# Kernel tuning notes

Hardware: AMD Instinct MI355X
Metric: run time of the kernel (lower is better)

## Reference

```python
import jax, jax.numpy as jnp
from jax import lax
import numpy as np

B, T, F_IN = 64, 3072, 128
CONV_OUT, K, STRIDE = 64, 3, 3
HID, OUT = 256, 10


def setup_inputs() -> dict:
    key = jax.random.key(0)
    ks = jax.random.split(key, 10)
    s = 0.05
    return {
        "input": jax.random.normal(ks[0], (B, T, F_IN), jnp.float32),
        "r": jnp.zeros(((T - K) // STRIDE + 1, B, CONV_OUT), jnp.float32),
        "hx0": jax.random.normal(ks[1], (B, HID), jnp.float32),
        "cx0": jax.random.normal(ks[2], (B, HID), jnp.float32),
        "conv_w": jax.random.normal(ks[3], (CONV_OUT, F_IN, K), jnp.float32) * s,
        "conv_b": jnp.zeros((CONV_OUT,), jnp.float32),
        "w_ih": jax.random.normal(ks[4], (4 * HID, CONV_OUT), jnp.float32) * s,
        "b_ih": jnp.zeros((4 * HID,), jnp.float32),
        "w_hh": jax.random.normal(ks[5], (4 * HID, HID), jnp.float32) * s,
        "b_hh": jnp.zeros((4 * HID,), jnp.float32),
        "lin_w": jax.random.normal(ks[6], (OUT, HID), jnp.float32) * s,
        "lin_b": jnp.zeros((OUT,), jnp.float32),
        "batch_size": B,
    }


def reference(input, r, hx0, cx0, conv_w, conv_b, w_ih, b_ih, w_hh, b_hh, lin_w, lin_b, batch_size):
    # F.normalize: L2 normalize along dim=1 (the time dim), eps=1e-12
    norm = jnp.sqrt(jnp.sum(input * input, axis=1, keepdims=True))
    x = input / jnp.maximum(norm, 1e-12)
    x = jnp.transpose(x, (0, 2, 1))  # [B, F_IN, T]
    x = lax.conv_general_dilated(
        x, conv_w, window_strides=(STRIDE,), padding='VALID',
        dimension_numbers=('NCH', 'OIH', 'NCH')) + conv_b[None, :, None]
    x = jax.nn.relu(x)
    x = jnp.transpose(x, (2, 0, 1))  # [T', B, 64]

    def step(carry, xt):
        h, c = carry
        gates = xt @ w_ih.T + b_ih + h @ w_hh.T + b_hh  # [B, 4H]
        i, f, g, o = jnp.split(gates, 4, axis=-1)
        c = jax.nn.sigmoid(f) * c + jax.nn.sigmoid(i) * jnp.tanh(g)
        h = jax.nn.sigmoid(o) * jnp.tanh(c)
        return (h, c), None

    (h, _), _ = lax.scan(step, (hx0, cx0), x)
    return h @ lin_w.T + lin_b  # [B, OUT]
```

## Files before the change

kernel.cpp:

```cpp
#include <hip/hip_runtime.h>
#include <math.h>

#define B_N 64
#define T_N 3072
#define FIN 128
#define TP 1024
#define COUT 64
#define HID 256
#define G4 1024
#define OUT_N 10
#define NCHUNK 24
#define CHUNK_T (T_N / NCHUNK)

#define WREG 24
#define WLDS 8

typedef _Float16 h2_t __attribute__((ext_vector_type(2)));
typedef unsigned u32x4 __attribute__((ext_vector_type(4)));

#if defined(__has_builtin)
#if __has_builtin(__builtin_amdgcn_fdot2)
#define HAVE_FDOT2 1
#endif
#endif

__device__ __forceinline__ float fdot2(unsigned w, unsigned h, float acc) {
#ifdef HAVE_FDOT2
    return __builtin_amdgcn_fdot2(__builtin_bit_cast(h2_t, w),
                                  __builtin_bit_cast(h2_t, h), acc, false);
#else
    h2_t wv = __builtin_bit_cast(h2_t, w), hv = __builtin_bit_cast(h2_t, h);
    return acc + (float)wv.x * (float)hv.x + (float)wv.y * (float)hv.y;
#endif
}

__device__ __forceinline__ unsigned pack2(float a, float b) {
    unsigned la = (unsigned)__builtin_bit_cast(unsigned short, (_Float16)a);
    unsigned lb = (unsigned)__builtin_bit_cast(unsigned short, (_Float16)b);
    return la | (lb << 16);
}

__global__ void pack_weights(const float* __restrict__ w_ih,
                             const float* __restrict__ w_hh,
                             unsigned* __restrict__ whhR,
                             unsigned* __restrict__ whhL,
                             float* __restrict__ wihT) {
    int col = blockIdx.x, d = threadIdx.x;
    const float* wr = w_hh + col * HID;
    unsigned p = pack2(wr[2 * d], wr[2 * d + 1]);
    int c = d >> 2, r = d & 3;
    if (c < WREG) whhR[(c * 1024 + col) * 4 + r] = p;
    else          whhL[((c - WREG) * 1024 + col) * 4 + r] = p;
    if (d < COUT) wihT[d * 1024 + col] = w_ih[col * COUT + d];
}

__global__ void prep_conv_w(const float* __restrict__ conv_w, float* __restrict__ wc2) {
    int i = blockIdx.x * 256 + threadIdx.x;
    if (i < 24576) {
        int j = i >> 6, oc = i & 63;
        int kk = j >> 7, ic = j & 127;
        wc2[i] = conv_w[(oc * 128 + ic) * 3 + kk];
    }
}

__global__ void norm_partial(const float* __restrict__ in, float* __restrict__ part) {
    int b = blockIdx.x, ch = blockIdx.y, f = threadIdx.x;
    const float* p = in + ((size_t)b * T_N + (size_t)ch * CHUNK_T) * FIN + f;
    float s0 = 0.f, s1 = 0.f, s2 = 0.f, s3 = 0.f;
#pragma unroll
    for (int r = 0; r < CHUNK_T; r += 4) {
        float v0 = p[(r + 0) * FIN];
        float v1 = p[(r + 1) * FIN];
        float v2 = p[(r + 2) * FIN];
        float v3 = p[(r + 3) * FIN];
        s0 += v0 * v0; s1 += v1 * v1; s2 += v2 * v2; s3 += v3 * v3;
    }
    part[(b * NCHUNK + ch) * FIN + f] = (s0 + s1) + (s2 + s3);
}

__global__ __launch_bounds__(256) void conv_relu(
        const float* __restrict__ in, const float* __restrict__ part,
        const float* __restrict__ wc2, const float* __restrict__ cb,
        float* __restrict__ X) {
    __shared__ __align__(16) float xs[16 * 384];
    __shared__ __align__(16) float wsh[96 * 64];
    __shared__ float invn[FIN];

    int b = blockIdx.x, tile = blockIdx.y;
    int tid = threadIdx.x;

    if (tid < FIN) {
        float s = 0.f;
#pragma unroll
        for (int c = 0; c < NCHUNK; c++) s += part[(b * NCHUNK + c) * FIN + tid];
        invn[tid] = rsqrtf(fmaxf(s, 1e-24f));
    }
    __syncthreads();

    const float* ip = in + ((size_t)b * T_N + (size_t)tile * 48) * FIN;
    for (int i = tid; i < 6144; i += 256) xs[i] = ip[i] * invn[i & 127];

    int oc = tid & 63, tq = tid >> 6;
    float acc0 = 0.f, acc1 = 0.f, acc2 = 0.f, acc3 = 0.f;
    const float* xb = xs + tq * 4 * 384;

    for (int c = 0; c < 4; c++) {
        __syncthreads();
        for (int i = tid; i < 6144; i += 256) wsh[i] = wc2[c * 6144 + i];
        __syncthreads();
#pragma unroll 8
        for (int jj = 0; jj < 96; jj += 4) {
            int j = c * 96 + jj;
            float w0 = wsh[(jj + 0) * 64 + oc];
            float w1 = wsh[(jj + 1) * 64 + oc];
            float w2 = wsh[(jj + 2) * 64 + oc];
            float w3 = wsh[(jj + 3) * 64 + oc];
            float4 x0 = *(const float4*)(xb + j);
            float4 x1 = *(const float4*)(xb + 384 + j);
            float4 x2 = *(const float4*)(xb + 768 + j);
            float4 x3 = *(const float4*)(xb + 1152 + j);
            acc0 += w0 * x0.x + w1 * x0.y + w2 * x0.z + w3 * x0.w;
            acc1 += w0 * x1.x + w1 * x1.y + w2 * x1.z + w3 * x1.w;
            acc2 += w0 * x2.x + w1 * x2.y + w2 * x2.z + w3 * x2.w;
            acc3 += w0 * x3.x + w1 * x3.y + w2 * x3.z + w3 * x3.w;
        }
    }
    float bb = cb[oc];
    int tp0 = tile * 16 + tq * 4;
    size_t o = ((size_t)b * TP + tp0) * COUT + oc;
    X[o]       = fmaxf(acc0 + bb, 0.f);
    X[o + 64]  = fmaxf(acc1 + bb, 0.f);
    X[o + 128] = fmaxf(acc2 + bb, 0.f);
    X[o + 192] = fmaxf(acc3 + bb, 0.f);
}

__global__ __launch_bounds__(256) void x_gemm(
        const float* __restrict__ X, const float* __restrict__ wihT,
        const float* __restrict__ b_ih, const float* __restrict__ b_hh,
        _Float16* __restrict__ xg) {
    __shared__ float xs[64 * 17];
    int b = blockIdx.x, t0 = blockIdx.y * 16, tid = threadIdx.x;

    const float* Xp = X + ((size_t)b * TP + t0) * COUT;
    for (int i = tid; i < 1024; i += 256) {
        int r = i >> 6, k = i & 63;
        xs[k * 17 + r] = Xp[i];
    }
    __syncthreads();

#pragma unroll
    for (int jt = 0; jt < 4; jt++) {
        int jj = jt * 256 + tid;
        float bias = b_ih[jj] + b_hh[jj];
        float acc[16];
#pragma unroll
        for (int r = 0; r < 16; r++) acc[r] = bias;
        for (int k = 0; k < 64; k++) {
            float w = wihT[k * 1024 + jj];
#pragma unroll
            for (int r = 0; r < 16; r++) acc[r] += w * xs[k * 17 + r];
        }
#pragma unroll
        for (int r = 0; r < 16; r++)
            xg[((size_t)b * TP + t0 + r) * 1024 + jj] = (_Float16)acc[r];
    }
}

__device__ __forceinline__ float fsig(float x) {
    return 1.f / (1.f + __expf(-x));
}
__device__ __forceinline__ float ftanh(float x) {
    float xc = fminf(fmaxf(x, -15.f), 15.f);
    float e = __expf(2.f * xc);
    return (e - 1.f) / (e + 1.f);
}

#define SM_WL   0
#define SM_H    131072
#define SM_FO   131584
#define SM_H32  133632
#define SM_SIZE 134656

#define REP24(M) M(0) M(1) M(2) M(3) M(4) M(5) M(6) M(7) M(8) M(9) M(10) M(11) \
                 M(12) M(13) M(14) M(15) M(16) M(17) M(18) M(19) M(20) M(21) M(22) M(23)
#define REP8(M)  M(0) M(1) M(2) M(3) M(4) M(5) M(6) M(7)

#define DECLW(n)  u32x4 wa##n, wb##n;
#define LOADW(n)  wa##n = whhR4[(n) * 1024 + j]; wb##n = whhR4[(n) * 1024 + j + 512];
#define DOTCH(n)  { u32x4 H = hs4[n]; \
    a0 = fdot2(wa##n[0], H[0], a0); a1 = fdot2(wb##n[0], H[0], a1); \
    a0 = fdot2(wa##n[1], H[1], a0); a1 = fdot2(wb##n[1], H[1], a1); \
    a0 = fdot2(wa##n[2], H[2], a0); a1 = fdot2(wb##n[2], H[2], a1); \
    a0 = fdot2(wa##n[3], H[3], a0); a1 = fdot2(wb##n[3], H[3], a1); }
#define DOTLDS(m) { u32x4 WA = wL[(m) * 1024 + j]; u32x4 WB = wL[(m) * 1024 + j + 512]; \
    u32x4 H = hs4[WREG + (m)]; \
    a0 = fdot2(WA[0], H[0], a0); a1 = fdot2(WB[0], H[0], a1); \
    a0 = fdot2(WA[1], H[1], a0); a1 = fdot2(WB[1], H[1], a1); \
    a0 = fdot2(WA[2], H[2], a0); a1 = fdot2(WB[2], H[2], a1); \
    a0 = fdot2(WA[3], H[3], a0); a1 = fdot2(WB[3], H[3], a1); }

__global__ __attribute__((amdgpu_flat_work_group_size(512, 512),
                          amdgpu_waves_per_eu(2, 2)))
void lstm_kernel(
        const u32x4* __restrict__ whhR4, const u32x4* __restrict__ whhL4,
        const _Float16* __restrict__ xg,
        const float* __restrict__ hx0, const float* __restrict__ cx0,
        const float* __restrict__ lin_w, const float* __restrict__ lin_b,
        float* __restrict__ out) {
    extern __shared__ char smem[];
    u32x4*    wL    = (u32x4*)(smem + SM_WL);
    _Float16* h_s   = (_Float16*)(smem + SM_H);
    float2*   fo_s  = (float2*)(smem + SM_FO);
    float*    h32_s = (float*)(smem + SM_H32);

    const int b = blockIdx.x, j = threadIdx.x;

    REP24(DECLW)
    REP24(LOADW)

    for (int i = j; i < WLDS * 1024; i += 512) wL[i] = whhL4[i];

    float c_reg = 0.f;
    if (j < HID) {
        c_reg = cx0[b * HID + j];
        h_s[j] = (_Float16)hx0[b * HID + j];
    }
    const _Float16* Xg = xg + (size_t)b * TP * G4;
    _Float16 xa = Xg[j], xb = Xg[j + 512];
    __syncthreads();

    const u32x4* hs4 = (const u32x4*)h_s;

    for (int t = 0; t < TP; t++) {
        _Float16 xan = (_Float16)0.f, xbn = (_Float16)0.f;
        if (t + 1 < TP) {
            xan = Xg[(t + 1) * G4 + j];
            xbn = Xg[(t + 1) * G4 + j + 512];
        }

        float a0 = (float)xa, a1 = (float)xb;
        REP24(DOTCH)
        REP8(DOTLDS)

        float s0 = 0.f, s1 = 0.f;
        if (j >= HID) {
            fo_s[j - HID] = make_float2(fsig(a0), fsig(a1));
        } else {
            s0 = fsig(a0);
            s1 = ftanh(a1);
        }
        __syncthreads();
        if (j < HID) {
            float2 fo = fo_s[j];
            c_reg = fo.x * c_reg + s0 * s1;
            float hh = fo.y * ftanh(c_reg);
            h_s[j] = (_Float16)hh;
            if (t == TP - 1) h32_s[j] = hh;
        }
        __syncthreads();
        xa = xan; xb = xbn;
    }

    if (j < OUT_N) {
        float s = lin_b[j];
        const float* lw = lin_w + j * HID;
#pragma unroll 4
        for (int k = 0; k < HID; k++) s += h32_s[k] * lw[k];
        out[b * OUT_N + j] = s;
    }
}

extern "C" void kernel_launch(void* const* d_in, const int* in_sizes, int n_in,
                              void* d_out, int out_size, void* d_ws, size_t ws_size,
                              hipStream_t stream) {
    const float* input  = (const float*)d_in[0];
    const float* hx0    = (const float*)d_in[2];
    const float* cx0    = (const float*)d_in[3];
    const float* conv_w = (const float*)d_in[4];
    const float* conv_b = (const float*)d_in[5];
    const float* w_ih   = (const float*)d_in[6];
    const float* b_ih   = (const float*)d_in[7];
    const float* w_hh   = (const float*)d_in[8];
    const float* b_hh   = (const float*)d_in[9];
    const float* lin_w  = (const float*)d_in[10];
    const float* lin_b  = (const float*)d_in[11];

    float* ws = (float*)d_ws;
    float*     part = ws;
    float*     X    = part + 196608;
    float*     wc2  = X + 4194304;
    float*     wihT = wc2 + 24576;
    unsigned*  whhR = (unsigned*)(wihT + 65536);
    unsigned*  whhL = whhR + WREG * 1024 * 4;
    _Float16*  xg   = (_Float16*)(whhL + WLDS * 1024 * 4);

    (void)hipFuncSetAttribute((const void*)lstm_kernel,
                              hipFuncAttributeMaxDynamicSharedMemorySize, SM_SIZE);

    pack_weights<<<1024, 128, 0, stream>>>(w_ih, w_hh, whhR, whhL, wihT);
    prep_conv_w<<<96, 256, 0, stream>>>(conv_w, wc2);
    norm_partial<<<dim3(B_N, NCHUNK), FIN, 0, stream>>>(input, part);
    conv_relu<<<dim3(B_N, 64), 256, 0, stream>>>(input, part, wc2, conv_b, X);
    x_gemm<<<dim3(B_N, 64), 256, 0, stream>>>(X, wihT, b_ih, b_hh, xg);
    lstm_kernel<<<B_N, 512, SM_SIZE, stream>>>(
        (const u32x4*)whhR, (const u32x4*)whhL, xg,
        hx0, cx0, lin_w, lin_b, (float*)d_out);
}
```

Baseline: 2.527 ms.

## Use 1024 threads per LSTM block, one gate column per thread, three-tier weight storage

New measurement: 2.586 ms. 2.3% more time.

```diff
diff --git a/kernel.cpp b/kernel.cpp
--- a/kernel.cpp
+++ b/kernel.cpp
@@ -12,8 +12,9 @@
 #define NCHUNK 24
 #define CHUNK_T (T_N / NCHUNK)
 
-#define WREG 24
-#define WLDS 8
+#define CREG 20
+#define CLDS 9
+#define CSTR 3
 
 typedef _Float16 h2_t __attribute__((ext_vector_type(2)));
 typedef unsigned u32x4 __attribute__((ext_vector_type(4)));
@@ -44,13 +45,15 @@
                              const float* __restrict__ w_hh,
                              unsigned* __restrict__ whhR,
                              unsigned* __restrict__ whhL,
+                             unsigned* __restrict__ whhS,
                              float* __restrict__ wihT) {
     int col = blockIdx.x, d = threadIdx.x;
     const float* wr = w_hh + col * HID;
     unsigned p = pack2(wr[2 * d], wr[2 * d + 1]);
     int c = d >> 2, r = d & 3;
-    if (c < WREG) whhR[(c * 1024 + col) * 4 + r] = p;
-    else          whhL[((c - WREG) * 1024 + col) * 4 + r] = p;
+    if (c < CREG)            whhR[((c) * 1024 + col) * 4 + r] = p;
+    else if (c < CREG + CLDS) whhL[((c - CREG) * 1024 + col) * 4 + r] = p;
+    else                     whhS[((c - CREG - CLDS) * 1024 + col) * 4 + r] = p;
     if (d < COUT) wihT[d * 1024 + col] = w_ih[col * COUT + d];
 }
 
@@ -176,33 +179,27 @@
 }
 
 #define SM_WL   0
-#define SM_H    131072
-#define SM_FO   131584
-#define SM_H32  133632
-#define SM_SIZE 134656
-
-#define REP24(M) M(0) M(1) M(2) M(3) M(4) M(5) M(6) M(7) M(8) M(9) M(10) M(11) \
-                 M(12) M(13) M(14) M(15) M(16) M(17) M(18) M(19) M(20) M(21) M(22) M(23)
-#define REP8(M)  M(0) M(1) M(2) M(3) M(4) M(5) M(6) M(7)
-
-#define DECLW(n)  u32x4 wa##n, wb##n;
-#define LOADW(n)  wa##n = whhR4[(n) * 1024 + j]; wb##n = whhR4[(n) * 1024 + j + 512];
-#define DOTCH(n)  { u32x4 H = hs4[n]; \
-    a0 = fdot2(wa##n[0], H[0], a0); a1 = fdot2(wb##n[0], H[0], a1); \
-    a0 = fdot2(wa##n[1], H[1], a0); a1 = fdot2(wb##n[1], H[1], a1); \
-    a0 = fdot2(wa##n[2], H[2], a0); a1 = fdot2(wb##n[2], H[2], a1); \
-    a0 = fdot2(wa##n[3], H[3], a0); a1 = fdot2(wb##n[3], H[3], a1); }
-#define DOTLDS(m) { u32x4 WA = wL[(m) * 1024 + j]; u32x4 WB = wL[(m) * 1024 + j + 512]; \
-    u32x4 H = hs4[WREG + (m)]; \
-    a0 = fdot2(WA[0], H[0], a0); a1 = fdot2(WB[0], H[0], a1); \
-    a0 = fdot2(WA[1], H[1], a0); a1 = fdot2(WB[1], H[1], a1); \
-    a0 = fdot2(WA[2], H[2], a0); a1 = fdot2(WB[2], H[2], a1); \
-    a0 = fdot2(WA[3], H[3], a0); a1 = fdot2(WB[3], H[3], a1); }
-
-__global__ __attribute__((amdgpu_flat_work_group_size(512, 512),
-                          amdgpu_waves_per_eu(2, 2)))
+#define SM_H    147456
+#define SM_GSH  147968
+#define SM_H32  151040
+#define SM_SIZE 152064
+
+#define REP20(M) M(0) M(1) M(2) M(3) M(4) M(5) M(6) M(7) M(8) M(9) \
+                 M(10) M(11) M(12) M(13) M(14) M(15) M(16) M(17) M(18) M(19)
+#define REP9(M)  M(0) M(1) M(2) M(3) M(4) M(5) M(6) M(7) M(8)
+
+#define DECLW(n)  u32x4 wr##n;
+#define LOADW(n)  wr##n = whhR4[(n) * 1024 + j];
+#define DOT4(W, H) { \
+    a0 = fdot2((W)[0], (H)[0], a0); a0 = fdot2((W)[1], (H)[1], a0); \
+    a0 = fdot2((W)[2], (H)[2], a0); a0 = fdot2((W)[3], (H)[3], a0); }
+#define DOTCH(n)  { u32x4 H = hs4[n]; DOT4(wr##n, H); }
+#define DOTLDS(m) { u32x4 W = wL[(m) * 1024 + j]; u32x4 H = hs4[CREG + (m)]; DOT4(W, H); }
+
+__global__ __attribute__((amdgpu_flat_work_group_size(1024, 1024)))
 void lstm_kernel(
         const u32x4* __restrict__ whhR4, const u32x4* __restrict__ whhL4,
+        const u32x4* __restrict__ whhS4,
         const _Float16* __restrict__ xg,
         const float* __restrict__ hx0, const float* __restrict__ cx0,
         const float* __restrict__ lin_w, const float* __restrict__ lin_b,
@@ -210,15 +207,15 @@
     extern __shared__ char smem[];
     u32x4*    wL    = (u32x4*)(smem + SM_WL);
     _Float16* h_s   = (_Float16*)(smem + SM_H);
-    float2*   fo_s  = (float2*)(smem + SM_FO);
+    float*    gsh   = (float*)(smem + SM_GSH);
     float*    h32_s = (float*)(smem + SM_H32);
 
     const int b = blockIdx.x, j = threadIdx.x;
 
-    REP24(DECLW)
-    REP24(LOADW)
-
-    for (int i = j; i < WLDS * 1024; i += 512) wL[i] = whhL4[i];
+    REP20(DECLW)
+    REP20(LOADW)
+
+    for (int i = j; i < CLDS * 1024; i += 1024) wL[i] = whhL4[i];
 
     float c_reg = 0.f;
     if (j < HID) {
@@ -226,39 +223,43 @@
         h_s[j] = (_Float16)hx0[b * HID + j];
     }
     const _Float16* Xg = xg + (size_t)b * TP * G4;
-    _Float16 xa = Xg[j], xb = Xg[j + 512];
+    _Float16 xa = Xg[j];
     __syncthreads();
 
     const u32x4* hs4 = (const u32x4*)h_s;
+    const u32x4* sP = whhS4 + j;
 
     for (int t = 0; t < TP; t++) {
-        _Float16 xan = (_Float16)0.f, xbn = (_Float16)0.f;
-        if (t + 1 < TP) {
-            xan = Xg[(t + 1) * G4 + j];
-            xbn = Xg[(t + 1) * G4 + j + 512];
+        _Float16 xan = (_Float16)0.f;
+        if (t + 1 < TP) xan = Xg[(t + 1) * G4 + j];
+
+        u32x4 s0 = sP[0 * 1024], s1 = sP[1 * 1024], s2 = sP[2 * 1024];
+
+        float a0 = (float)xa;
+        REP20(DOTCH)
+        REP9(DOTLDS)
+        { u32x4 H = hs4[29]; DOT4(s0, H); }
+        { u32x4 H = hs4[30]; DOT4(s1, H); }
+        { u32x4 H = hs4[31]; DOT4(s2, H); }
+
+        if (j >= HID) {
+            float v;
+            if (j < 512)      v = fsig(a0);
+            else if (j < 768) v = ftanh(a0);
+            else              v = fsig(a0);
+            gsh[j - HID] = v;
         }
-
-        float a0 = (float)xa, a1 = (float)xb;
-        REP24(DOTCH)
-        REP8(DOTLDS)
-
-        float s0 = 0.f, s1 = 0.f;
-        if (j >= HID) {
-            fo_s[j - HID] = make_float2(fsig(a0), fsig(a1));
-        } else {
-            s0 = fsig(a0);
-            s1 = ftanh(a1);
-        }
+        float ig = fsig(a0);
         __syncthreads();
         if (j < HID) {
-            float2 fo = fo_s[j];
-            c_reg = fo.x * c_reg + s0 * s1;
-            float hh = fo.y * ftanh(c_reg);
+            float fg = gsh[j], gg = gsh[HID + j], og = gsh[2 * HID + j];
+            c_reg = fg * c_reg + ig * gg;
+            float hh = og * ftanh(c_reg);
             h_s[j] = (_Float16)hh;
             if (t == TP - 1) h32_s[j] = hh;
         }
         __syncthreads();
-        xa = xan; xb = xbn;
+        xa = xan;
     }
 
     if (j < OUT_N) {
@@ -291,18 +292,19 @@
     float*     wc2  = X + 4194304;
     float*     wihT = wc2 + 24576;
     unsigned*  whhR = (unsigned*)(wihT + 65536);
-    unsigned*  whhL = whhR + WREG * 1024 * 4;
-    _Float16*  xg   = (_Float16*)(whhL + WLDS * 1024 * 4);
+    unsigned*  whhL = whhR + CREG * 1024 * 4;
+    unsigned*  whhS = whhL + CLDS * 1024 * 4;
+    _Float16*  xg   = (_Float16*)(whhS + CSTR * 1024 * 4);
 
     (void)hipFuncSetAttribute((const void*)lstm_kernel,
                               hipFuncAttributeMaxDynamicSharedMemorySize, SM_SIZE);
 
-    pack_weights<<<1024, 128, 0, stream>>>(w_ih, w_hh, whhR, whhL, wihT);
+    pack_weights<<<1024, 128, 0, stream>>>(w_ih, w_hh, whhR, whhL, whhS, wihT);
     prep_conv_w<<<96, 256, 0, stream>>>(conv_w, wc2);
     norm_partial<<<dim3(B_N, NCHUNK), FIN, 0, stream>>>(input, part);
     conv_relu<<<dim3(B_N, 64), 256, 0, stream>>>(input, part, wc2, conv_b, X);
     x_gemm<<<dim3(B_N, 64), 256, 0, stream>>>(X, wihT, b_ih, b_hh, xg);
-    lstm_kernel<<<B_N, 512, SM_SIZE, stream>>>(
-        (const u32x4*)whhR, (const u32x4*)whhL, xg,
+    lstm_kernel<<<B_N, 1024, SM_SIZE, stream>>>(
+        (const u32x4*)whhR, (const u32x4*)whhL, (const u32x4*)whhS, xg,
         hx0, cx0, lin_w, lin_b, (float*)d_out);
 }
```

## Hold recurrent weights in AGPRs so W_hh splits VGPR/AGPR/LDS evenly

Applied to the files above, without the earlier changes.

Measured after the change: 3.030 ms. 19.9% more time.

```diff
diff --git a/kernel.cpp b/kernel.cpp
--- a/kernel.cpp
+++ b/kernel.cpp
@@ -12,8 +12,6 @@
 #define NCHUNK 24
 #define CHUNK_T (T_N / NCHUNK)
 
-#define WREG 24
-#define WLDS 8
 
 typedef _Float16 h2_t __attribute__((ext_vector_type(2)));
 typedef unsigned u32x4 __attribute__((ext_vector_type(4)));
@@ -42,15 +40,22 @@
 
 __global__ void pack_weights(const float* __restrict__ w_ih,
                              const float* __restrict__ w_hh,
-                             unsigned* __restrict__ whhR,
+                             unsigned* __restrict__ whhV,
+                             unsigned* __restrict__ whhA,
                              unsigned* __restrict__ whhL,
                              float* __restrict__ wihT) {
     int col = blockIdx.x, d = threadIdx.x;
     const float* wr = w_hh + col * HID;
     unsigned p = pack2(wr[2 * d], wr[2 * d + 1]);
     int c = d >> 2, r = d & 3;
-    if (c < WREG) whhR[(c * 1024 + col) * 4 + r] = p;
-    else          whhL[((c - WREG) * 1024 + col) * 4 + r] = p;
+    if (col < 512) {
+        if (c < 16) whhV[((c) * 512 + col) * 4 + r] = p;
+        else        whhA[((c - 16) * 512 + col) * 4 + r] = p;
+    } else {
+        int jj = col - 512;
+        if (c < 16) whhA[((16 + c) * 512 + jj) * 4 + r] = p;
+        else        whhL[((c - 16) * 512 + jj) * 4 + r] = p;
+    }
     if (d < COUT) wihT[d * 1024 + col] = w_ih[col * COUT + d];
 }
 
@@ -175,50 +180,76 @@
     return (e - 1.f) / (e + 1.f);
 }
 
-#define SM_WL   0
+#define SM_WLB  0
 #define SM_H    131072
 #define SM_FO   131584
 #define SM_H32  133632
 #define SM_SIZE 134656
 
-#define REP24(M) M(0) M(1) M(2) M(3) M(4) M(5) M(6) M(7) M(8) M(9) M(10) M(11) \
-                 M(12) M(13) M(14) M(15) M(16) M(17) M(18) M(19) M(20) M(21) M(22) M(23)
-#define REP8(M)  M(0) M(1) M(2) M(3) M(4) M(5) M(6) M(7)
-
-#define DECLW(n)  u32x4 wa##n, wb##n;
-#define LOADW(n)  wa##n = whhR4[(n) * 1024 + j]; wb##n = whhR4[(n) * 1024 + j + 512];
-#define DOTCH(n)  { u32x4 H = hs4[n]; \
-    a0 = fdot2(wa##n[0], H[0], a0); a1 = fdot2(wb##n[0], H[0], a1); \
-    a0 = fdot2(wa##n[1], H[1], a0); a1 = fdot2(wb##n[1], H[1], a1); \
-    a0 = fdot2(wa##n[2], H[2], a0); a1 = fdot2(wb##n[2], H[2], a1); \
-    a0 = fdot2(wa##n[3], H[3], a0); a1 = fdot2(wb##n[3], H[3], a1); }
-#define DOTLDS(m) { u32x4 WA = wL[(m) * 1024 + j]; u32x4 WB = wL[(m) * 1024 + j + 512]; \
-    u32x4 H = hs4[WREG + (m)]; \
-    a0 = fdot2(WA[0], H[0], a0); a1 = fdot2(WB[0], H[0], a1); \
-    a0 = fdot2(WA[1], H[1], a0); a1 = fdot2(WB[1], H[1], a1); \
-    a0 = fdot2(WA[2], H[2], a0); a1 = fdot2(WB[2], H[2], a1); \
-    a0 = fdot2(WA[3], H[3], a0); a1 = fdot2(WB[3], H[3], a1); }
-
-__global__ __attribute__((amdgpu_flat_work_group_size(512, 512),
-                          amdgpu_waves_per_eu(2, 2)))
-void lstm_kernel(
-        const u32x4* __restrict__ whhR4, const u32x4* __restrict__ whhL4,
+#define REP16(M) M(0) M(1) M(2) M(3) M(4) M(5) M(6) M(7) \
+                 M(8) M(9) M(10) M(11) M(12) M(13) M(14) M(15)
+
+#define DECLV(n)  u32x4 wr##n;
+#define LOADV(n)  wr##n = whhV4[(n) * 512 + j];
+#define PINV(n)   asm volatile("" : "+v"(wr##n));
+
+#define DECLAG(n) unsigned ag##n##_0, ag##n##_1, ag##n##_2, ag##n##_3, \
+                           bg##n##_0, bg##n##_1, bg##n##_2, bg##n##_3;
+#define INITAG(n) { u32x4 v = whhA4[(n) * 512 + j]; \
+    asm volatile("v_accvgpr_write_b32 %0, %1" : "=a"(ag##n##_0) : "v"(v[0])); \
+    asm volatile("v_accvgpr_write_b32 %0, %1" : "=a"(ag##n##_1) : "v"(v[1])); \
+    asm volatile("v_accvgpr_write_b32 %0, %1" : "=a"(ag##n##_2) : "v"(v[2])); \
+    asm volatile("v_accvgpr_write_b32 %0, %1" : "=a"(ag##n##_3) : "v"(v[3])); \
+    v = whhA4[(16 + (n)) * 512 + j]; \
+    asm volatile("v_accvgpr_write_b32 %0, %1" : "=a"(bg##n##_0) : "v"(v[0])); \
+    asm volatile("v_accvgpr_write_b32 %0, %1" : "=a"(bg##n##_1) : "v"(v[1])); \
+    asm volatile("v_accvgpr_write_b32 %0, %1" : "=a"(bg##n##_2) : "v"(v[2])); \
+    asm volatile("v_accvgpr_write_b32 %0, %1" : "=a"(bg##n##_3) : "v"(v[3])); }
+
+#define DOT_LO(n) { u32x4 H = hs4[n]; \
+    a0 = fdot2(wr##n[0], H[0], a0); a0 = fdot2(wr##n[1], H[1], a0); \
+    a0 = fdot2(wr##n[2], H[2], a0); a0 = fdot2(wr##n[3], H[3], a0); \
+    unsigned w0, w1, w2, w3; \
+    asm volatile("v_accvgpr_read_b32 %0, %1" : "=v"(w0) : "a"(bg##n##_0)); \
+    asm volatile("v_accvgpr_read_b32 %0, %1" : "=v"(w1) : "a"(bg##n##_1)); \
+    asm volatile("v_accvgpr_read_b32 %0, %1" : "=v"(w2) : "a"(bg##n##_2)); \
+    asm volatile("v_accvgpr_read_b32 %0, %1" : "=v"(w3) : "a"(bg##n##_3)); \
+    a1 = fdot2(w0, H[0], a1); a1 = fdot2(w1, H[1], a1); \
+    a1 = fdot2(w2, H[2], a1); a1 = fdot2(w3, H[3], a1); }
+
+#define DOT_HI(n) { u32x4 H = hs4[16 + (n)]; \
+    unsigned w0, w1, w2, w3; \
+    asm volatile("v_accvgpr_read_b32 %0, %1" : "=v"(w0) : "a"(ag##n##_0)); \
+    asm volatile("v_accvgpr_read_b32 %0, %1" : "=v"(w1) : "a"(ag##n##_1)); \
+    asm volatile("v_accvgpr_read_b32 %0, %1" : "=v"(w2) : "a"(ag##n##_2)); \
+    asm volatile("v_accvgpr_read_b32 %0, %1" : "=v"(w3) : "a"(ag##n##_3)); \
+    a0 = fdot2(w0, H[0], a0); a0 = fdot2(w1, H[1], a0); \
+    a0 = fdot2(w2, H[2], a0); a0 = fdot2(w3, H[3], a0); \
+    u32x4 W = wLB4[(n) * 512 + j]; \
+    a1 = fdot2(W[0], H[0], a1); a1 = fdot2(W[1], H[1], a1); \
+    a1 = fdot2(W[2], H[2], a1); a1 = fdot2(W[3], H[3], a1); }
+
+__global__ __launch_bounds__(512) void lstm_kernel(
+        const u32x4* __restrict__ whhV4, const u32x4* __restrict__ whhA4,
+        const u32x4* __restrict__ whhL4,
         const _Float16* __restrict__ xg,
         const float* __restrict__ hx0, const float* __restrict__ cx0,
         const float* __restrict__ lin_w, const float* __restrict__ lin_b,
         float* __restrict__ out) {
     extern __shared__ char smem[];
-    u32x4*    wL    = (u32x4*)(smem + SM_WL);
+    u32x4*    wLB4  = (u32x4*)(smem + SM_WLB);
     _Float16* h_s   = (_Float16*)(smem + SM_H);
     float2*   fo_s  = (float2*)(smem + SM_FO);
     float*    h32_s = (float*)(smem + SM_H32);
 
     const int b = blockIdx.x, j = threadIdx.x;
 
-    REP24(DECLW)
-    REP24(LOADW)
-
-    for (int i = j; i < WLDS * 1024; i += 512) wL[i] = whhL4[i];
+    REP16(DECLV)
+    REP16(LOADV)
+    REP16(PINV)
+    REP16(DECLAG)
+    REP16(INITAG)
+    for (int i = j; i < 16 * 512; i += 512) wLB4[i] = whhL4[i];
 
     float c_reg = 0.f;
     if (j < HID) {
@@ -226,39 +257,34 @@
         h_s[j] = (_Float16)hx0[b * HID + j];
     }
     const _Float16* Xg = xg + (size_t)b * TP * G4;
-    _Float16 xa = Xg[j], xb = Xg[j + 512];
+    _Float16 xa0 = Xg[j], xa1 = Xg[j + 512];
     __syncthreads();
 
     const u32x4* hs4 = (const u32x4*)h_s;
 
+#pragma unroll 1
     for (int t = 0; t < TP; t++) {
-        _Float16 xan = (_Float16)0.f, xbn = (_Float16)0.f;
+        _Float16 xn0 = (_Float16)0.f, xn1 = (_Float16)0.f;
         if (t + 1 < TP) {
-            xan = Xg[(t + 1) * G4 + j];
-            xbn = Xg[(t + 1) * G4 + j + 512];
+            xn0 = Xg[(t + 1) * G4 + j];
+            xn1 = Xg[(t + 1) * G4 + j + 512];
         }
 
-        float a0 = (float)xa, a1 = (float)xb;
-        REP24(DOTCH)
-        REP8(DOTLDS)
-
-        float s0 = 0.f, s1 = 0.f;
-        if (j >= HID) {
-            fo_s[j - HID] = make_float2(fsig(a0), fsig(a1));
-        } else {
-            s0 = fsig(a0);
-            s1 = ftanh(a1);
-        }
+        float a0 = (float)xa0, a1 = (float)xa1;
+        REP16(DOT_LO)
+        REP16(DOT_HI)
+
+        if (j >= HID) fo_s[j - HID] = make_float2(fsig(a0), fsig(a1));
         __syncthreads();
         if (j < HID) {
             float2 fo = fo_s[j];
-            c_reg = fo.x * c_reg + s0 * s1;
+            c_reg = fo.x * c_reg + fsig(a0) * ftanh(a1);
             float hh = fo.y * ftanh(c_reg);
             h_s[j] = (_Float16)hh;
             if (t == TP - 1) h32_s[j] = hh;
         }
         __syncthreads();
-        xa = xan; xb = xbn;
+        xa0 = xn0; xa1 = xn1;
     }
 
     if (j < OUT_N) {
@@ -290,19 +316,20 @@
     float*     X    = part + 196608;
     float*     wc2  = X + 4194304;
     float*     wihT = wc2 + 24576;
-    unsigned*  whhR = (unsigned*)(wihT + 65536);
-    unsigned*  whhL = whhR + WREG * 1024 * 4;
-    _Float16*  xg   = (_Float16*)(whhL + WLDS * 1024 * 4);
+    unsigned*  whhV = (unsigned*)(wihT + 65536);
+    unsigned*  whhA = whhV + 32768;
+    unsigned*  whhL = whhA + 65536;
+    _Float16*  xg   = (_Float16*)(whhL + 32768);
 
     (void)hipFuncSetAttribute((const void*)lstm_kernel,
                               hipFuncAttributeMaxDynamicSharedMemorySize, SM_SIZE);
 
-    pack_weights<<<1024, 128, 0, stream>>>(w_ih, w_hh, whhR, whhL, wihT);
+    pack_weights<<<1024, 128, 0, stream>>>(w_ih, w_hh, whhV, whhA, whhL, wihT);
     prep_conv_w<<<96, 256, 0, stream>>>(conv_w, wc2);
     norm_partial<<<dim3(B_N, NCHUNK), FIN, 0, stream>>>(input, part);
     conv_relu<<<dim3(B_N, 64), 256, 0, stream>>>(input, part, wc2, conv_b, X);
     x_gemm<<<dim3(B_N, 64), 256, 0, stream>>>(X, wihT, b_ih, b_hh, xg);
     lstm_kernel<<<B_N, 512, SM_SIZE, stream>>>(
-        (const u32x4*)whhR, (const u32x4*)whhL, xg,
+        (const u32x4*)whhV, (const u32x4*)whhA, (const u32x4*)whhL, xg,
         hx0, cx0, lin_w, lin_b, (float*)d_out);
 }
```
